# Kernel tuning notes

Measured on AMD Instinct MI355X. Metric: run time of the kernel, lower is better.

## Reference

```python
import jax, jax.numpy as jnp
import numpy as np

NUM_EXPERTS = 64
TOP_K = 2
NOISE_STD = 0.1


def setup_inputs() -> dict:
    key = jax.random.key(0)
    k1, k2, k3 = jax.random.split(key, 3)
    x = jax.random.normal(k1, (8192, 4096), dtype=jnp.float32)
    W = jax.random.normal(k2, (NUM_EXPERTS, 4096), dtype=jnp.float32) * 0.01  # nn.init.normal_(std=0.01)
    noise = jax.random.normal(k3, (8192, NUM_EXPERTS), dtype=jnp.float32)
    return {"x": x, "W": W, "noise": noise}


def reference(x, W, noise):
    batch = x.shape[0]
    # router_logits = x @ W^T  -> [batch, num_experts]
    router_logits = jnp.einsum("bd,ed->be", x, W)
    noisy_logits = router_logits + NOISE_STD * noise  # training=True path
    top_k_logits, top_k_indices = jax.lax.top_k(noisy_logits, TOP_K)
    expert_weights = jax.nn.softmax(top_k_logits, axis=-1)
    # load balancing loss (Switch Transformer): one_hot(sel).sum over k and batch
    # replaced by scatter-add counts per expert
    counts = jnp.zeros((NUM_EXPERTS,), dtype=jnp.float32).at[top_k_indices.reshape(-1)].add(1.0)
    fraction_tokens = counts / batch
    router_probs = jax.nn.softmax(router_logits, axis=-1)
    mean_router_prob = router_probs.mean(axis=0)
    load_balance_loss = NUM_EXPERTS * jnp.sum(fraction_tokens * mean_router_prob)
    return (top_k_indices, expert_weights, router_logits, load_balance_loss)
```

## Files before the change

### kernel.cpp

```cpp
#include <hip/hip_runtime.h>
#include <hip/hip_bf16.h>

#define BATCH 8192
#define DMODEL 4096
#define NEXP 64

typedef __attribute__((ext_vector_type(8))) short short8;
typedef __attribute__((ext_vector_type(4))) float f32x4;

#define WF_USHORTS 786432
#define WF_FLOATS  393216

#define GLD16(dst_lds, src_g)                                                  \
    __builtin_amdgcn_global_load_lds(                                          \
        (const __attribute__((address_space(1))) void*)(src_g),                \
        (__attribute__((address_space(3))) void*)(dst_lds), 16, 0, 0)

__global__ __launch_bounds__(256) void build_wf(const float* __restrict__ W,
                                                unsigned short* __restrict__ WF2)
{
    const int gid = blockIdx.x * 256 + threadIdx.x;
    const int ks = gid >> 8;
    const int cf = (gid >> 6) & 3;
    const int l  = gid & 63;
    const int e  = cf * 16 + (l & 15);
    const int k0 = ks * 32 + (l >> 4) * 8;
    const float* src = W + (size_t)e * DMODEL + k0;

    const size_t base = (size_t)ks * 6144 + cf * 512 + l * 8;
#pragma unroll
    for (int j = 0; j < 8; ++j) {
        const float xv = src[j];
        const __hip_bfloat16 h = __float2bfloat16(xv);
        const float r1 = xv - __bfloat162float(h);
        const __hip_bfloat16 m = __float2bfloat16(r1);
        const float r2 = r1 - __bfloat162float(m);
        const __hip_bfloat16 lo = __float2bfloat16(r2);
        WF2[base + j]        = __builtin_bit_cast(unsigned short, h);
        WF2[base + 2048 + j] = __builtin_bit_cast(unsigned short, m);
        WF2[base + 4096 + j] = __builtin_bit_cast(unsigned short, lo);
    }
}


#define CVT1(V, J, AH, AM, AL) {                                              \
    const float xv_ = (V);                                                    \
    const __hip_bfloat16 h_ = __float2bfloat16(xv_);                          \
    const float r1_ = xv_ - __bfloat162float(h_);                             \
    const __hip_bfloat16 m_ = __float2bfloat16(r1_);                          \
    const float r2_ = r1_ - __bfloat162float(m_);                             \
    const __hip_bfloat16 l_ = __float2bfloat16(r2_);                          \
    AH[J] = (short)__builtin_bit_cast(unsigned short, h_);                    \
    AM[J] = (short)__builtin_bit_cast(unsigned short, m_);                    \
    AL[J] = (short)__builtin_bit_cast(unsigned short, l_); }

#define CVT8(X0, X1, AH, AM, AL)                                              \
    CVT1(X0[0], 0, AH, AM, AL) CVT1(X0[1], 1, AH, AM, AL)                     \
    CVT1(X0[2], 2, AH, AM, AL) CVT1(X0[3], 3, AH, AM, AL)                     \
    CVT1(X1[0], 4, AH, AM, AL) CVT1(X1[1], 5, AH, AM, AL)                     \
    CVT1(X1[2], 6, AH, AM, AL) CVT1(X1[3], 7, AH, AM, AL)

#define MFMA(A, B, C) __builtin_amdgcn_mfma_f32_16x16x32_bf16(A, B, C, 0, 0, 0)

__global__ __launch_bounds__(256, 2) void gemm_mfma(const float* __restrict__ x,
                                                    const unsigned short* __restrict__ WF2,
                                                    float* __restrict__ part,
                                                    int S)
{
    __shared__ float xs[2][4096];
    __shared__ unsigned short wsh[2][6144];

    const int t = threadIdx.x;
    const int l = t & 63;
    const int wid = t >> 6;
    const int g = blockIdx.x & 63;
    const int s = blockIdx.x >> 6;
    const int rowbase = g * 128;
    const int kbeg = s * (DMODEL / S);
    const int nsteps = (DMODEL / S) >> 5;

    const float* pxa[4];
#pragma unroll
    for (int r = 0; r < 4; ++r) {
        const int tr = wid * 32 + r * 8 + (l >> 3);
        const int ul = (l & 7) ^ (tr & 7);
        pxa[r] = x + (size_t)(rowbase + tr) * DMODEL + kbeg + ul * 4;
    }
    const unsigned short* pwb = WF2 + (size_t)(kbeg >> 5) * 6144 + t * 8;

#define STAGE(BUF, IT) {                                                       \
    _Pragma("unroll")                                                          \
    for (int r_ = 0; r_ < 4; ++r_)                                             \
        GLD16(&xs[BUF][wid * 1024 + r_ * 256], pxa[r_] + (size_t)(IT) * 32);   \
    _Pragma("unroll")                                                          \
    for (int r_ = 0; r_ < 3; ++r_)                                             \
        GLD16(&wsh[BUF][r_ * 2048 + wid * 512],                                \
              pwb + (size_t)(IT) * 6144 + r_ * 2048); }

    const int lr = l & 15;
    const int lk = l >> 4;
    const int xr = lr & 7;
    const int tr0 = wid * 32 + lr;
    const int tr1 = tr0 + 16;
    const int a00 = tr0 * 32 + (((lk * 2)     ^ xr) * 4);
    const int a01 = tr0 * 32 + (((lk * 2 + 1) ^ xr) * 4);
    const int a10 = tr1 * 32 + (((lk * 2)     ^ xr) * 4);
    const int a11 = tr1 * 32 + (((lk * 2 + 1) ^ xr) * 4);

    f32x4 acc[2][4] = {};

    STAGE(0, 0)

    for (int it = 0; it < nsteps; ++it) {
        const int cur = it & 1;
        if (it + 1 < nsteps) {
            STAGE(cur ^ 1, it + 1)
            asm volatile("s_waitcnt vmcnt(7)" ::: "memory");
        } else {
            asm volatile("s_waitcnt vmcnt(0)" ::: "memory");
        }
        __builtin_amdgcn_s_barrier();

        const f32x4 xa0 = *(const f32x4*)&xs[cur][a00];
        const f32x4 xa1 = *(const f32x4*)&xs[cur][a01];
        const f32x4 xb0 = *(const f32x4*)&xs[cur][a10];
        const f32x4 xb1 = *(const f32x4*)&xs[cur][a11];
        short8 ah0, am0, al0, ah1, am1, al1;
        CVT8(xa0, xa1, ah0, am0, al0)
        CVT8(xb0, xb1, ah1, am1, al1)

#pragma unroll
        for (int cf = 0; cf < 4; ++cf) {
            const unsigned short* wp = &wsh[cur][cf * 512 + l * 8];
            const short8 bh = *(const short8*)(wp);
            const short8 bm = *(const short8*)(wp + 2048);
            const short8 bl = *(const short8*)(wp + 4096);
            acc[0][cf] = MFMA(ah0, bh, acc[0][cf]);
            acc[1][cf] = MFMA(ah1, bh, acc[1][cf]);
            acc[0][cf] = MFMA(ah0, bm, acc[0][cf]);
            acc[1][cf] = MFMA(ah1, bm, acc[1][cf]);
            acc[0][cf] = MFMA(am0, bh, acc[0][cf]);
            acc[1][cf] = MFMA(am1, bh, acc[1][cf]);
            acc[0][cf] = MFMA(ah0, bl, acc[0][cf]);
            acc[1][cf] = MFMA(ah1, bl, acc[1][cf]);
            acc[0][cf] = MFMA(al0, bh, acc[0][cf]);
            acc[1][cf] = MFMA(al1, bh, acc[1][cf]);
            acc[0][cf] = MFMA(am0, bm, acc[0][cf]);
            acc[1][cf] = MFMA(am1, bm, acc[1][cf]);
        }
        __builtin_amdgcn_s_barrier();
    }

    const int orow = lk * 4;
#pragma unroll
    for (int rf = 0; rf < 2; ++rf)
#pragma unroll
        for (int j = 0; j < 4; ++j) {
            const int row = rowbase + wid * 32 + rf * 16 + orow + j;
            float* dst = part + ((size_t)s * BATCH + row) * NEXP + lr;
#pragma unroll
            for (int cf = 0; cf < 4; ++cf)
                dst[cf * 16] = acc[rf][cf][j];
        }
#undef STAGE
}

template<int NS>
__global__ __launch_bounds__(256) void router2(const float* __restrict__ part,
                                               const float* __restrict__ noise,
                                               float* __restrict__ out,
                                               float* __restrict__ probsum,
                                               float* __restrict__ counts)
{
    __shared__ float sps[4][64];
    __shared__ float scnt[4][64];

    const int t = threadIdx.x;
    const int w = t >> 6;
    const int lane = t & 63;
    const int wg = blockIdx.x * 4 + w;

    float* out_idx = out;
    float* out_w = out + 16384;
    float* out_logits = out + 32768;

    float psum_local = 0.f;
    float cnt_local = 0.f;

    for (int r = 0; r < 8; ++r) {
        const int row = wg * 8 + r;
        float lgt = 0.f;
#pragma unroll
        for (int s = 0; s < NS; ++s)
            lgt += part[((size_t)s * BATCH + row) * NEXP + lane];
        out_logits[(size_t)row * NEXP + lane] = lgt;

        const float ny = lgt + 0.1f * noise[(size_t)row * NEXP + lane];

        float v1 = ny; int i1 = lane;
#pragma unroll
        for (int m = 32; m >= 1; m >>= 1) {
            float ov = __shfl_xor(v1, m);
            int oi = __shfl_xor(i1, m);
            if (ov > v1 || (ov == v1 && oi < i1)) { v1 = ov; i1 = oi; }
        }
        float v2 = (lane == i1) ? -1e30f : ny; int i2 = lane;
#pragma unroll
        for (int m = 32; m >= 1; m >>= 1) {
            float ov = __shfl_xor(v2, m);
            int oi = __shfl_xor(i2, m);
            if (ov > v2 || (ov == v2 && oi < i2)) { v2 = ov; i2 = oi; }
        }

        if (lane == 0) {
            const float d = expf(v2 - v1);
            const float w1 = 1.0f / (1.0f + d);
            out_idx[row * 2 + 0] = (float)i1;
            out_idx[row * 2 + 1] = (float)i2;
            out_w[row * 2 + 0] = w1;
            out_w[row * 2 + 1] = 1.0f - w1;
        }

        float m = lgt;
#pragma unroll
        for (int ss = 32; ss >= 1; ss >>= 1) m = fmaxf(m, __shfl_xor(m, ss));
        const float p = expf(lgt - m);
        float sum = p;
#pragma unroll
        for (int ss = 32; ss >= 1; ss >>= 1) sum += __shfl_xor(sum, ss);
        psum_local += p / sum;
        cnt_local += (lane == i1 ? 1.f : 0.f) + (lane == i2 ? 1.f : 0.f);
    }

    sps[w][lane] = psum_local;
    scnt[w][lane] = cnt_local;
    __syncthreads();
    if (t < 64) {
        float ssum = 0.f, c = 0.f;
#pragma unroll
        for (int ww = 0; ww < 4; ++ww) { ssum += sps[ww][t]; c += scnt[ww][t]; }
        atomicAdd(&probsum[t], ssum);
        atomicAdd(&counts[t], c);
    }
}

__global__ void loss_kernel(const float* __restrict__ probsum,
                            const float* __restrict__ counts,
                            float* __restrict__ out_loss)
{
    const int e = threadIdx.x;
    float v = probsum[e] * counts[e];
#pragma unroll
    for (int s = 32; s >= 1; s >>= 1) v += __shfl_xor(v, s);
    if (e == 0)
        out_loss[0] = (float)NEXP * v / ((float)BATCH * (float)BATCH);
}

extern "C" void kernel_launch(void* const* d_in, const int* in_sizes, int n_in,
                              void* d_out, int out_size, void* d_ws, size_t ws_size,
                              hipStream_t stream)
{
    const float* x = (const float*)d_in[0];
    const float* W = (const float*)d_in[1];
    const float* noise = (const float*)d_in[2];
    float* out = (float*)d_out;
    float* ws = (float*)d_ws;

    float* probsum = ws;
    float* counts = ws + 64;
    unsigned short* WF2 = (unsigned short*)(ws + 256);
    float* part = ws + 256 + WF_FLOATS;

    int S = 1;
    const size_t base_floats = 256 + WF_FLOATS;
    for (int cand = 8; cand >= 1; cand >>= 1) {
        const size_t need = (base_floats + (size_t)cand * BATCH * NEXP) * sizeof(float);
        if (ws_size >= need) { S = cand; break; }
    }

    hipMemsetAsync(d_ws, 0, 512, stream);

    build_wf<<<128, 256, 0, stream>>>(W, WF2);
    gemm_mfma<<<64 * S, 256, 0, stream>>>(x, WF2, part, S);
    switch (S) {
        case 8: router2<8><<<256, 256, 0, stream>>>(part, noise, out, probsum, counts); break;
        case 4: router2<4><<<256, 256, 0, stream>>>(part, noise, out, probsum, counts); break;
        case 2: router2<2><<<256, 256, 0, stream>>>(part, noise, out, probsum, counts); break;
        default: router2<1><<<256, 256, 0, stream>>>(part, noise, out, probsum, counts); break;
    }
    loss_kernel<<<1, 64, 0, stream>>>(probsum, counts, out + 557056);
}
```

Measured before the change: 64.44 us.

## Halve GEMM row tile, raise occupancy, vectorize W stores, fuse loss into router

The GEMM row tile per block drops from 128 to 64 rows (16 per wave), the grid doubles and launch bounds now request 4 blocks per CU, so the LDS and register footprint shrink and more waves can hide latency. The W split-to-bf16 prep kernel now writes its three parts as 16-byte vector stores instead of scalar ones. The separate loss kernel is removed: the last router block, found with an atomic counter, computes the load-balance loss, which saves one launch. Smaller tiles mean less reuse of the W fragments per load and more x/W traffic per FLOP.

```diff
diff --git a/kernel.cpp b/kernel.cpp
--- a/kernel.cpp
+++ b/kernel.cpp
@@ -8,7 +8,6 @@
 typedef __attribute__((ext_vector_type(8))) short short8;
 typedef __attribute__((ext_vector_type(4))) float f32x4;
 
-#define WF_USHORTS 786432
 #define WF_FLOATS  393216
 
 #define GLD16(dst_lds, src_g)                                                  \
@@ -27,7 +26,7 @@
     const int k0 = ks * 32 + (l >> 4) * 8;
     const float* src = W + (size_t)e * DMODEL + k0;
 
-    const size_t base = (size_t)ks * 6144 + cf * 512 + l * 8;
+    short8 hv, mv, lv;
 #pragma unroll
     for (int j = 0; j < 8; ++j) {
         const float xv = src[j];
@@ -36,10 +35,14 @@
         const __hip_bfloat16 m = __float2bfloat16(r1);
         const float r2 = r1 - __bfloat162float(m);
         const __hip_bfloat16 lo = __float2bfloat16(r2);
-        WF2[base + j]        = __builtin_bit_cast(unsigned short, h);
-        WF2[base + 2048 + j] = __builtin_bit_cast(unsigned short, m);
-        WF2[base + 4096 + j] = __builtin_bit_cast(unsigned short, lo);
-    }
+        hv[j] = (short)__builtin_bit_cast(unsigned short, h);
+        mv[j] = (short)__builtin_bit_cast(unsigned short, m);
+        lv[j] = (short)__builtin_bit_cast(unsigned short, lo);
+    }
+    const size_t base = (size_t)ks * 6144 + cf * 512 + l * 8;
+    *(short8*)&WF2[base]        = hv;
+    *(short8*)&WF2[base + 2048] = mv;
+    *(short8*)&WF2[base + 4096] = lv;
 }
 
 
@@ -62,27 +65,27 @@
 
 #define MFMA(A, B, C) __builtin_amdgcn_mfma_f32_16x16x32_bf16(A, B, C, 0, 0, 0)
 
-__global__ __launch_bounds__(256, 2) void gemm_mfma(const float* __restrict__ x,
+__global__ __launch_bounds__(256, 4) void gemm_mfma(const float* __restrict__ x,
                                                     const unsigned short* __restrict__ WF2,
                                                     float* __restrict__ part,
                                                     int S)
 {
-    __shared__ float xs[2][4096];
+    __shared__ float xs[2][2048];
     __shared__ unsigned short wsh[2][6144];
 
     const int t = threadIdx.x;
     const int l = t & 63;
     const int wid = t >> 6;
-    const int g = blockIdx.x & 63;
-    const int s = blockIdx.x >> 6;
-    const int rowbase = g * 128;
+    const int g = blockIdx.x & 127;
+    const int s = blockIdx.x >> 7;
+    const int rowbase = g * 64;
     const int kbeg = s * (DMODEL / S);
     const int nsteps = (DMODEL / S) >> 5;
 
-    const float* pxa[4];
-#pragma unroll
-    for (int r = 0; r < 4; ++r) {
-        const int tr = wid * 32 + r * 8 + (l >> 3);
+    const float* pxa[2];
+#pragma unroll
+    for (int r = 0; r < 2; ++r) {
+        const int tr = wid * 16 + r * 8 + (l >> 3);
         const int ul = (l & 7) ^ (tr & 7);
         pxa[r] = x + (size_t)(rowbase + tr) * DMODEL + kbeg + ul * 4;
     }
@@ -90,8 +93,8 @@
 
 #define STAGE(BUF, IT) {                                                       \
     _Pragma("unroll")                                                          \
-    for (int r_ = 0; r_ < 4; ++r_)                                             \
-        GLD16(&xs[BUF][wid * 1024 + r_ * 256], pxa[r_] + (size_t)(IT) * 32);   \
+    for (int r_ = 0; r_ < 2; ++r_)                                             \
+        GLD16(&xs[BUF][wid * 512 + r_ * 256], pxa[r_] + (size_t)(IT) * 32);    \
     _Pragma("unroll")                                                          \
     for (int r_ = 0; r_ < 3; ++r_)                                             \
         GLD16(&wsh[BUF][r_ * 2048 + wid * 512],                                \
@@ -100,14 +103,11 @@
     const int lr = l & 15;
     const int lk = l >> 4;
     const int xr = lr & 7;
-    const int tr0 = wid * 32 + lr;
-    const int tr1 = tr0 + 16;
-    const int a00 = tr0 * 32 + (((lk * 2)     ^ xr) * 4);
-    const int a01 = tr0 * 32 + (((lk * 2 + 1) ^ xr) * 4);
-    const int a10 = tr1 * 32 + (((lk * 2)     ^ xr) * 4);
-    const int a11 = tr1 * 32 + (((lk * 2 + 1) ^ xr) * 4);
-
-    f32x4 acc[2][4] = {};
+    const int trw = wid * 16 + lr;
+    const int a0 = trw * 32 + (((lk * 2)     ^ xr) * 4);
+    const int a1 = trw * 32 + (((lk * 2 + 1) ^ xr) * 4);
+
+    f32x4 acc[4] = {};
 
     STAGE(0, 0)
 
@@ -115,19 +115,16 @@
         const int cur = it & 1;
         if (it + 1 < nsteps) {
             STAGE(cur ^ 1, it + 1)
-            asm volatile("s_waitcnt vmcnt(7)" ::: "memory");
+            asm volatile("s_waitcnt vmcnt(5)" ::: "memory");
         } else {
             asm volatile("s_waitcnt vmcnt(0)" ::: "memory");
         }
         __builtin_amdgcn_s_barrier();
 
-        const f32x4 xa0 = *(const f32x4*)&xs[cur][a00];
-        const f32x4 xa1 = *(const f32x4*)&xs[cur][a01];
-        const f32x4 xb0 = *(const f32x4*)&xs[cur][a10];
-        const f32x4 xb1 = *(const f32x4*)&xs[cur][a11];
-        short8 ah0, am0, al0, ah1, am1, al1;
-        CVT8(xa0, xa1, ah0, am0, al0)
-        CVT8(xb0, xb1, ah1, am1, al1)
+        const f32x4 xa0 = *(const f32x4*)&xs[cur][a0];
+        const f32x4 xa1 = *(const f32x4*)&xs[cur][a1];
+        short8 ah, am, al;
+        CVT8(xa0, xa1, ah, am, al)
 
 #pragma unroll
         for (int cf = 0; cf < 4; ++cf) {
@@ -135,33 +132,25 @@
             const short8 bh = *(const short8*)(wp);
             const short8 bm = *(const short8*)(wp + 2048);
             const short8 bl = *(const short8*)(wp + 4096);
-            acc[0][cf] = MFMA(ah0, bh, acc[0][cf]);
-            acc[1][cf] = MFMA(ah1, bh, acc[1][cf]);
-            acc[0][cf] = MFMA(ah0, bm, acc[0][cf]);
-            acc[1][cf] = MFMA(ah1, bm, acc[1][cf]);
-            acc[0][cf] = MFMA(am0, bh, acc[0][cf]);
-            acc[1][cf] = MFMA(am1, bh, acc[1][cf]);
-            acc[0][cf] = MFMA(ah0, bl, acc[0][cf]);
-            acc[1][cf] = MFMA(ah1, bl, acc[1][cf]);
-            acc[0][cf] = MFMA(al0, bh, acc[0][cf]);
-            acc[1][cf] = MFMA(al1, bh, acc[1][cf]);
-            acc[0][cf] = MFMA(am0, bm, acc[0][cf]);
-            acc[1][cf] = MFMA(am1, bm, acc[1][cf]);
+            acc[cf] = MFMA(ah, bh, acc[cf]);
+            acc[cf] = MFMA(ah, bm, acc[cf]);
+            acc[cf] = MFMA(am, bh, acc[cf]);
+            acc[cf] = MFMA(ah, bl, acc[cf]);
+            acc[cf] = MFMA(al, bh, acc[cf]);
+            acc[cf] = MFMA(am, bm, acc[cf]);
         }
         __builtin_amdgcn_s_barrier();
     }
 
     const int orow = lk * 4;
 #pragma unroll
-    for (int rf = 0; rf < 2; ++rf)
-#pragma unroll
-        for (int j = 0; j < 4; ++j) {
-            const int row = rowbase + wid * 32 + rf * 16 + orow + j;
-            float* dst = part + ((size_t)s * BATCH + row) * NEXP + lr;
-#pragma unroll
-            for (int cf = 0; cf < 4; ++cf)
-                dst[cf * 16] = acc[rf][cf][j];
-        }
+    for (int j = 0; j < 4; ++j) {
+        const int row = rowbase + wid * 16 + orow + j;
+        float* dst = part + ((size_t)s * BATCH + row) * NEXP + lr;
+#pragma unroll
+        for (int cf = 0; cf < 4; ++cf)
+            dst[cf * 16] = acc[cf][j];
+    }
 #undef STAGE
 }
 
@@ -170,10 +159,12 @@
                                                const float* __restrict__ noise,
                                                float* __restrict__ out,
                                                float* __restrict__ probsum,
-                                               float* __restrict__ counts)
+                                               float* __restrict__ counts,
+                                               int* __restrict__ done)
 {
     __shared__ float sps[4][64];
     __shared__ float scnt[4][64];
+    __shared__ int lastFlag;
 
     const int t = threadIdx.x;
     const int w = t >> 6;
@@ -242,18 +233,23 @@
         atomicAdd(&probsum[t], ssum);
         atomicAdd(&counts[t], c);
     }
-}
-
-__global__ void loss_kernel(const float* __restrict__ probsum,
-                            const float* __restrict__ counts,
-                            float* __restrict__ out_loss)
-{
-    const int e = threadIdx.x;
-    float v = probsum[e] * counts[e];
-#pragma unroll
-    for (int s = 32; s >= 1; s >>= 1) v += __shfl_xor(v, s);
-    if (e == 0)
-        out_loss[0] = (float)NEXP * v / ((float)BATCH * (float)BATCH);
+    __syncthreads();
+    if (t == 0) {
+        __threadfence();
+        lastFlag = (atomicAdd(done, 1) == (int)gridDim.x - 1) ? 1 : 0;
+    }
+    __syncthreads();
+    if (lastFlag && t < 64) {
+        const float ps = __hip_atomic_load(&probsum[t], __ATOMIC_RELAXED,
+                                           __HIP_MEMORY_SCOPE_AGENT);
+        const float ct = __hip_atomic_load(&counts[t], __ATOMIC_RELAXED,
+                                           __HIP_MEMORY_SCOPE_AGENT);
+        float v = ps * ct;
+#pragma unroll
+        for (int ss = 32; ss >= 1; ss >>= 1) v += __shfl_xor(v, ss);
+        if (t == 0)
+            out[557056] = (float)NEXP * v / ((float)BATCH * (float)BATCH);
+    }
 }
 
 extern "C" void kernel_launch(void* const* d_in, const int* in_sizes, int n_in,
@@ -268,6 +264,7 @@
 
     float* probsum = ws;
     float* counts = ws + 64;
+    int* done = (int*)(ws + 128);
     unsigned short* WF2 = (unsigned short*)(ws + 256);
     float* part = ws + 256 + WF_FLOATS;
 
@@ -278,15 +275,14 @@
         if (ws_size >= need) { S = cand; break; }
     }
 
-    hipMemsetAsync(d_ws, 0, 512, stream);
+    hipMemsetAsync(d_ws, 0, 1024, stream);
 
     build_wf<<<128, 256, 0, stream>>>(W, WF2);
-    gemm_mfma<<<64 * S, 256, 0, stream>>>(x, WF2, part, S);
+    gemm_mfma<<<128 * S, 256, 0, stream>>>(x, WF2, part, S);
     switch (S) {
-        case 8: router2<8><<<256, 256, 0, stream>>>(part, noise, out, probsum, counts); break;
-        case 4: router2<4><<<256, 256, 0, stream>>>(part, noise, out, probsum, counts); break;
-        case 2: router2<2><<<256, 256, 0, stream>>>(part, noise, out, probsum, counts); break;
-        default: router2<1><<<256, 256, 0, stream>>>(part, noise, out, probsum, counts); break;
-    }
-    loss_kernel<<<1, 64, 0, stream>>>(probsum, counts, out + 557056);
-}
+        case 8: router2<8><<<256, 256, 0, stream>>>(part, noise, out, probsum, counts, done); break;
+        case 4: router2<4><<<256, 256, 0, stream>>>(part, noise, out, probsum, counts, done); break;
+        case 2: router2<2><<<256, 256, 0, stream>>>(part, noise, out, probsum, counts, done); break;
+        default: router2<1><<<256, 256, 0, stream>>>(part, noise, out, probsum, counts, done); break;
+    }
+}
```

New measurement: 65.45 us. No clear change (+1.6%).
